# Performance work log

Measured on AMD Instinct MI355X. Metric: run time of the kernel, lower is better.

Reference implementation:

```python
import jax, jax.numpy as jnp
import numpy as np


def setup_inputs() -> dict:
    key = jax.random.key(0)
    ks = jax.random.split(key, 6)
    B, L, D, H, U = 256, 225, 1280, 256, 256
    features = jax.random.normal(ks[0], (B, L, D), dtype=jnp.float32)
    hidden = jax.random.normal(ks[1], (B, H), dtype=jnp.float32)
    W1 = jax.random.normal(ks[2], (D, U), dtype=jnp.float32) * (1.0 / np.sqrt(D))
    b1 = jnp.zeros((U,), dtype=jnp.float32)
    W2 = jax.random.normal(ks[3], (H, U), dtype=jnp.float32) * (1.0 / np.sqrt(H))
    b2 = jnp.zeros((U,), dtype=jnp.float32)
    V = jax.random.normal(ks[4], (U, 1), dtype=jnp.float32) * (1.0 / np.sqrt(U))
    bV = jnp.zeros((1,), dtype=jnp.float32)
    return {"features": features, "hidden": hidden, "W1": W1, "b1": b1,
            "W2": W2, "b2": b2, "V": V, "bV": bV}


def reference(features, hidden, W1, b1, W2, b2, V, bV):
    # features: [B, L, D]; hidden: [B, H]
    proj_f = jnp.einsum('bld,du->blu', features, W1) + b1        # [B, L, U]
    proj_h = (hidden @ W2 + b2)[:, None, :]                      # [B, 1, U]
    score = jnp.tanh(proj_f + proj_h)                            # [B, L, U]
    logits = jnp.einsum('blu,uo->blo', score, V) + bV            # [B, L, 1]
    attn = jax.nn.softmax(logits, axis=1)                        # [B, L, 1]
    context = jnp.sum(attn * features, axis=1)                   # [B, D]
    return context
```

## Files before the change

kernel.cpp:

```cpp
#include <hip/hip_runtime.h>
#include <hip/hip_bf16.h>

#define B_ 256
#define L_ 225
#define D_ 1280
#define H_ 256
#define U_ 256

typedef __bf16  bf16x8 __attribute__((ext_vector_type(8)));
typedef float   f32x4  __attribute__((ext_vector_type(4)));
typedef unsigned short u16x8 __attribute__((ext_vector_type(8)));

__device__ __forceinline__ unsigned short f2bf(float f) {
    union { __hip_bfloat16 h; unsigned short u; } cv;
    cv.h = __float2bfloat16(f);
    return cv.u;
}

__device__ __forceinline__ void gload_lds16(const void* g, void* l) {
    __builtin_amdgcn_global_load_lds(
        (const __attribute__((address_space(1))) unsigned int*)g,
        (__attribute__((address_space(3))) unsigned int*)l,
        16, 0, 0);
}

__device__ __forceinline__ float wredsum(float x) {
#pragma unroll
    for (int off = 32; off > 0; off >>= 1) x += __shfl_xor(x, off, 64);
    return x;
}

__global__ void k_prep(const float* __restrict__ W1,
                       const float* __restrict__ hidden,
                       const float* __restrict__ W2,
                       const float* __restrict__ b1,
                       const float* __restrict__ b2,
                       __hip_bfloat16* __restrict__ w1t,
                       float* __restrict__ ph) {
    int bid = blockIdx.x;
    if (bid < 1280) {
        int idx = bid * 256 + threadIdx.x;
        int k = idx / U_;
        int u = idx % U_;
        w1t[(size_t)u * D_ + k] = __float2bfloat16(W1[idx]);
    } else {
        __shared__ float sh[H_];
        int b = bid - 1280;
        int u = threadIdx.x;
        sh[u] = hidden[b * H_ + u];
        __syncthreads();
        float acc = b1[u] + b2[u];
#pragma unroll 8
        for (int h = 0; h < H_; ++h) acc += sh[h] * W2[h * U_ + u];
        ph[b * U_ + u] = acc;
    }
}

__global__ __launch_bounds__(1024, 4) void k_fused(
        const float* __restrict__ feat,
        const __hip_bfloat16* __restrict__ w1t,
        const float* __restrict__ ph,
        const float* __restrict__ Vv,
        float* __restrict__ out) {
    __shared__ __align__(128) char smem[138304];
    float* sV   = (float*)(smem + 131072);
    float* sPh  = (float*)(smem + 132096);
    float* sL   = (float*)(smem + 133120);
    float* sW   = (float*)(smem + 137216);
    float* sRed = (float*)(smem + 138240);

    const int tid  = threadIdx.x;
    const int lane = tid & 63;
    const int wave = tid >> 6;
    const int wr   = wave >> 2;
    const int wc   = wave & 3;
    const int b    = blockIdx.x;

    if (tid < 256) { sV[tid] = Vv[tid]; sPh[tid] = ph[b * 256 + tid]; }

    const int ar    = tid >> 2;
    const int arc   = ar < L_ ? ar : (L_ - 1);
    const int akseg = (tid & 3) << 4;
    const float* aSrc0 = feat + ((size_t)(b * L_ + arc) * D_ + akseg);
    const int ac80 = akseg >> 3;
    const int aswz = (ar & 7) << 4;

    f32x4 acc[4][4];
#pragma unroll
    for (int mi = 0; mi < 4; ++mi)
#pragma unroll
        for (int ni = 0; ni < 4; ++ni)
            acc[mi][ni] = (f32x4){0.f, 0.f, 0.f, 0.f};

    auto loadA = [&](int kt, f32x4* v) {
        const float* src = aSrc0 + kt * 64;
        v[0] = *reinterpret_cast<const f32x4*>(src);
        v[1] = *reinterpret_cast<const f32x4*>(src + 4);
        v[2] = *reinterpret_cast<const f32x4*>(src + 8);
        v[3] = *reinterpret_cast<const f32x4*>(src + 12);
    };
    auto stageB = [&](int kt, char* bufB) {
#pragma unroll
        for (int pass = 0; pass < 2; ++pass) {
            int s   = pass * 1024 + tid;
            int u   = s >> 3;
            int c8s = s & 7;
            int c8g = c8s ^ (u & 7);
            gload_lds16(w1t + (size_t)u * D_ + kt * 64 + c8g * 8, bufB + s * 16);
        }
    };
    auto storeA = [&](const f32x4* v, char* bufA) {
        u16x8 w0, w1;
        w0[0] = f2bf(v[0][0]); w0[1] = f2bf(v[0][1]); w0[2] = f2bf(v[0][2]); w0[3] = f2bf(v[0][3]);
        w0[4] = f2bf(v[1][0]); w0[5] = f2bf(v[1][1]); w0[6] = f2bf(v[1][2]); w0[7] = f2bf(v[1][3]);
        w1[0] = f2bf(v[2][0]); w1[1] = f2bf(v[2][1]); w1[2] = f2bf(v[2][2]); w1[3] = f2bf(v[2][3]);
        w1[4] = f2bf(v[3][0]); w1[5] = f2bf(v[3][1]); w1[6] = f2bf(v[3][2]); w1[7] = f2bf(v[3][3]);
        *reinterpret_cast<u16x8*>(bufA + (ar << 7) + ((ac80 << 4) ^ aswz))       = w0;
        *reinterpret_cast<u16x8*>(bufA + (ar << 7) + (((ac80 + 1) << 4) ^ aswz)) = w1;
    };
    auto compute = [&](const char* bufA, const char* bufB) {
#pragma unroll
        for (int ks = 0; ks < 2; ++ks) {
            const int kk2 = (ks * 32 + ((lane >> 4) << 3)) * 2;
            bf16x8 a[4], bb[4];
#pragma unroll
            for (int mi = 0; mi < 4; ++mi) {
                int r = wr * 64 + mi * 16 + (lane & 15);
                a[mi] = *reinterpret_cast<const bf16x8*>(bufA + (r << 7) + (kk2 ^ ((r & 7) << 4)));
            }
#pragma unroll
            for (int ni = 0; ni < 4; ++ni) {
                int u = wc * 64 + ni * 16 + (lane & 15);
                bb[ni] = *reinterpret_cast<const bf16x8*>(bufB + (u << 7) + (kk2 ^ ((u & 7) << 4)));
            }
#pragma unroll
            for (int mi = 0; mi < 4; ++mi)
#pragma unroll
                for (int ni = 0; ni < 4; ++ni)
                    acc[mi][ni] = __builtin_amdgcn_mfma_f32_16x16x32_bf16(
                        a[mi], bb[ni], acc[mi][ni], 0, 0, 0);
        }
    };

    {
        f32x4 v[4];
        loadA(0, v);
        stageB(0, smem + 32768);
        storeA(v, smem);
    }
    __syncthreads();
    int cur = 0;
    for (int kt = 0; kt < 20; ++kt) {
        char* bufN = smem + (cur ^ 1) * 65536;
        f32x4 v[4];
        if (kt < 19) { loadA(kt + 1, v); stageB(kt + 1, bufN + 32768); }
        char* bufC = smem + cur * 65536;
        compute(bufC, bufC + 32768);
        if (kt < 19) storeA(v, bufN);
        __syncthreads();
        cur ^= 1;
    }

    float phu[4], vu[4];
#pragma unroll
    for (int ni = 0; ni < 4; ++ni) {
        int u = wc * 64 + ni * 16 + (lane & 15);
        phu[ni] = sPh[u];
        vu[ni]  = sV[u];
    }
#pragma unroll
    for (int mi = 0; mi < 4; ++mi) {
#pragma unroll
        for (int rg = 0; rg < 4; ++rg) {
            int row = wr * 64 + mi * 16 + ((lane >> 4) << 2) + rg;
            float s = 0.f;
#pragma unroll
            for (int ni = 0; ni < 4; ++ni) {
                float x = acc[mi][ni][rg] + phu[ni];
                s += (1.f - 2.f / (__expf(2.f * x) + 1.f)) * vu[ni];
            }
            s += __shfl_xor(s, 1, 64);
            s += __shfl_xor(s, 2, 64);
            s += __shfl_xor(s, 4, 64);
            s += __shfl_xor(s, 8, 64);
            if ((lane & 15) == 0) sL[wc * 256 + row] = s;
        }
    }
    __syncthreads();
    float den_p = 0.f;
    if (tid < 256) {
        float lg = sL[tid] + sL[256 + tid] + sL[512 + tid] + sL[768 + tid];
        float w  = (tid < L_) ? __expf(lg) : 0.f;
        sW[tid] = w;
        den_p = w;
    }
    den_p = wredsum(den_p);
    if (lane == 0) sRed[wave] = den_p;
    __syncthreads();

    f32x4 c[5];
#pragma unroll
    for (int ch = 0; ch < 5; ++ch) c[ch] = (f32x4){0.f, 0.f, 0.f, 0.f};
    {
        const float* fB = feat + (size_t)b * L_ * D_;
        int l = wave;
        for (; l + 16 < L_; l += 32) {
            float wa = sW[l], wb = sW[l + 16];
            const float* ra = fB + (size_t)l * D_ + (lane << 2);
            const float* rb = fB + (size_t)(l + 16) * D_ + (lane << 2);
#pragma unroll
            for (int ch = 0; ch < 5; ++ch) {
                c[ch] += wa * *reinterpret_cast<const f32x4*>(ra + ch * 256);
                c[ch] += wb * *reinterpret_cast<const f32x4*>(rb + ch * 256);
            }
        }
        if (l < L_) {
            float wa = sW[l];
            const float* ra = fB + (size_t)l * D_ + (lane << 2);
#pragma unroll
            for (int ch = 0; ch < 5; ++ch)
                c[ch] += wa * *reinterpret_cast<const f32x4*>(ra + ch * 256);
        }
    }

    float* pc = (float*)smem;
#pragma unroll
    for (int ch = 0; ch < 5; ++ch)
        *reinterpret_cast<f32x4*>(pc + wave * 1280 + ch * 256 + (lane << 2)) = c[ch];
    __syncthreads();
    if (tid < 320) {
        f32x4 s = (f32x4){0.f, 0.f, 0.f, 0.f};
#pragma unroll
        for (int w = 0; w < 16; ++w)
            s += *reinterpret_cast<const f32x4*>(pc + w * 1280 + (tid << 2));
        float den = 0.f;
#pragma unroll
        for (int i = 0; i < 16; ++i) den += sRed[i];
        s *= (1.f / den);
        *reinterpret_cast<f32x4*>(out + (size_t)b * D_ + (tid << 2)) = s;
    }
}

extern "C" void kernel_launch(void* const* d_in, const int* in_sizes, int n_in,
                              void* d_out, int out_size, void* d_ws, size_t ws_size,
                              hipStream_t stream) {
    const float* feat   = (const float*)d_in[0];
    const float* hidden = (const float*)d_in[1];
    const float* W1     = (const float*)d_in[2];
    const float* b1     = (const float*)d_in[3];
    const float* W2     = (const float*)d_in[4];
    const float* b2     = (const float*)d_in[5];
    const float* Vv     = (const float*)d_in[6];

    char* ws = (char*)d_ws;
    __hip_bfloat16* w1t = (__hip_bfloat16*)(ws);
    float* ph = (float*)(ws + 655360);
    float* out = (float*)d_out;

    k_prep <<<1536, 256, 0, stream>>>(W1, hidden, W2, b1, b2, w1t, ph);
    k_fused<<<B_, 1024, 0, stream>>>(feat, w1t, ph, Vv, out);
}
```

Before: 127.5 us.

## Tile W1 transpose through shared memory and split context accumulation loop

The W1 transpose in the prep kernel now stages 64x64 tiles in padded shared memory, so reads and bf16 writes are both coalesced instead of scattered strided writes, and the prep grid shrinks accordingly. The context accumulation loop is split into two passes over L: first chunks 1-4 with one row per iteration, then chunk 0 in a second pass. The second pass likely targets cache reuse of rows still resident from the first pass, but it reissues loads over the feature rows and drops the two-row unrolling.

After: 126.8 us. About the same (-0.5%).

```diff
diff --git a/kernel.cpp b/kernel.cpp
--- a/kernel.cpp
+++ b/kernel.cpp
@@ -38,14 +38,27 @@
                        __hip_bfloat16* __restrict__ w1t,
                        float* __restrict__ ph) {
     int bid = blockIdx.x;
-    if (bid < 1280) {
-        int idx = bid * 256 + threadIdx.x;
-        int k = idx / U_;
-        int u = idx % U_;
-        w1t[(size_t)u * D_ + k] = __float2bfloat16(W1[idx]);
+    if (bid < 80) {
+        __shared__ float tile[64][65];
+        const int kt = bid >> 2;
+        const int ut = bid & 3;
+        const int k0 = kt * 64, u0 = ut * 64;
+        const int w  = threadIdx.x >> 6;
+        const int l  = threadIdx.x & 63;
+#pragma unroll
+        for (int i = 0; i < 16; ++i) {
+            int row = w * 16 + i;
+            tile[row][l] = W1[(size_t)(k0 + row) * U_ + u0 + l];
+        }
+        __syncthreads();
+#pragma unroll
+        for (int i = 0; i < 16; ++i) {
+            int urow = w * 16 + i;
+            w1t[(size_t)(u0 + urow) * D_ + k0 + l] = __float2bfloat16(tile[l][urow]);
+        }
     } else {
         __shared__ float sh[H_];
-        int b = bid - 1280;
+        int b = bid - 80;
         int u = threadIdx.x;
         sh[u] = hidden[b * H_ + u];
         __syncthreads();
@@ -202,24 +215,16 @@
 #pragma unroll
     for (int ch = 0; ch < 5; ++ch) c[ch] = (f32x4){0.f, 0.f, 0.f, 0.f};
     {
-        const float* fB = feat + (size_t)b * L_ * D_;
-        int l = wave;
-        for (; l + 16 < L_; l += 32) {
-            float wa = sW[l], wb = sW[l + 16];
-            const float* ra = fB + (size_t)l * D_ + (lane << 2);
-            const float* rb = fB + (size_t)(l + 16) * D_ + (lane << 2);
-#pragma unroll
-            for (int ch = 0; ch < 5; ++ch) {
+        const float* fB = feat + (size_t)b * L_ * D_ + (lane << 2);
+        for (int l = wave; l < L_; l += 16) {
+            float wa = sW[l];
+            const float* ra = fB + (size_t)l * D_;
+#pragma unroll
+            for (int ch = 1; ch < 5; ++ch)
                 c[ch] += wa * *reinterpret_cast<const f32x4*>(ra + ch * 256);
-                c[ch] += wb * *reinterpret_cast<const f32x4*>(rb + ch * 256);
-            }
-        }
-        if (l < L_) {
-            float wa = sW[l];
-            const float* ra = fB + (size_t)l * D_ + (lane << 2);
-#pragma unroll
-            for (int ch = 0; ch < 5; ++ch)
-                c[ch] += wa * *reinterpret_cast<const f32x4*>(ra + ch * 256);
+        }
+        for (int l = wave; l < L_; l += 16) {
+            c[0] += sW[l] * *reinterpret_cast<const f32x4*>(fB + (size_t)l * D_);
         }
     }
 
@@ -257,6 +262,6 @@
     float* ph = (float*)(ws + 655360);
     float* out = (float*)d_out;
 
-    k_prep <<<1536, 256, 0, stream>>>(W1, hidden, W2, b1, b2, w1t, ph);
+    k_prep <<<336, 256, 0, stream>>>(W1, hidden, W2, b1, b2, w1t, ph);
     k_fused<<<B_, 1024, 0, stream>>>(feat, w1t, ph, Vv, out);
 }
```
